# Kernel optimization log

Hardware: AMD Instinct MI355X
Metric: run time of the kernel (lower is better)

Reference implementation:

```python
import jax, jax.numpy as jnp
import numpy as np

E, K, H, I = 64, 8, 2048, 768  # num_experts, top_k, hidden, moe_intermediate

def setup_inputs() -> dict:
    key = jax.random.key(0)
    k1, k2, k3, k4 = jax.random.split(key, 4)
    return {
        "hidden_states": jax.random.normal(k1, (1, 1024, H), dtype=jnp.float32),
        "w_gate": jax.random.normal(k2, (H, E), dtype=jnp.float32) * 0.02,
        "w13": jax.random.normal(k3, (E, H, 2 * I), dtype=jnp.float32) * 0.02,  # fused gate+up proj
        "w2": jax.random.normal(k4, (E, I, H), dtype=jnp.float32) * 0.02,
    }

def reference(hidden_states, w_gate, w13, w2):
    orig_shape = hidden_states.shape
    x = hidden_states.reshape(-1, orig_shape[-1])            # [T, H]
    T = x.shape[0]

    # Router: logits -> softmax -> top-k -> renormalize (norm_topk_prob=True)
    router_logits = x @ w_gate                               # [T, E]
    probs = jax.nn.softmax(router_logits, axis=-1)
    topk_w, topk_idx = jax.lax.top_k(probs, K)               # [T, K]
    topk_w = topk_w / jnp.sum(topk_w, axis=-1, keepdims=True)
    # Dense combine-weight matrix [T, E] (zero for non-routed experts)
    combine = jnp.zeros((T, E), dtype=x.dtype).at[
        jnp.arange(T)[:, None], topk_idx].add(topk_w)

    # Expert SwiGLU FFN, computed densely for all experts, masked by combine
    h = jnp.einsum('th,ehd->etd', x, w13)                    # [E, T, 2I]
    gate, up = h[..., :I], h[..., I:]
    act = jax.nn.silu(gate) * up                             # [E, T, I]
    y = jnp.einsum('eti,eih->eth', act, w2)                  # [E, T, H]
    out = jnp.einsum('eth,te->th', y, combine)               # [T, H]
    return out.reshape(orig_shape)
```

## Files before the change

### kernel.cpp

```cpp
#include <hip/hip_runtime.h>
#include <hip/hip_bf16.h>
#include <math.h>

#define NE 64
#define NK 8
#define NH 2048
#define NI 768
#define NT 1024
#define BP 40
#define SUB64 (64 * BP)
#define SUB128 (128 * BP)

typedef float f32x4 __attribute__((ext_vector_type(4)));
typedef __bf16 bf16x8 __attribute__((ext_vector_type(8)));
typedef __bf16 bf16x4 __attribute__((ext_vector_type(4)));

__global__ __launch_bounds__(256) void router_k(
    const float* __restrict__ x, const float* __restrict__ wg,
    __bf16* __restrict__ x_bf, int* __restrict__ topk_idx,
    float* __restrict__ topk_w)
{
    __shared__ float xs[4][NH];
    const int wave = threadIdx.x >> 6;
    const int lane = threadIdx.x & 63;
    const int t = blockIdx.x * 4 + wave;

    const float* xrow = x + (size_t)t * NH;
    __bf16* brow = x_bf + (size_t)t * NH;
    #pragma unroll
    for (int j = 0; j < 8; ++j) {
        int idx = j * 256 + lane * 4;
        f32x4 v = *reinterpret_cast<const f32x4*>(xrow + idx);
        *reinterpret_cast<f32x4*>(&xs[wave][idx]) = v;
        bf16x4 b;
        b[0] = (__bf16)v.x; b[1] = (__bf16)v.y; b[2] = (__bf16)v.z; b[3] = (__bf16)v.w;
        *reinterpret_cast<bf16x4*>(brow + idx) = b;
    }
    __syncthreads();

    float a0 = 0.f, a1 = 0.f, a2 = 0.f, a3 = 0.f;
    for (int h = 0; h < NH; h += 4) {
        a0 = fmaf(xs[wave][h + 0], wg[(h + 0) * NE + lane], a0);
        a1 = fmaf(xs[wave][h + 1], wg[(h + 1) * NE + lane], a1);
        a2 = fmaf(xs[wave][h + 2], wg[(h + 2) * NE + lane], a2);
        a3 = fmaf(xs[wave][h + 3], wg[(h + 3) * NE + lane], a3);
    }
    float acc = (a0 + a1) + (a2 + a3);

    float cur = acc;
    float sel_v[NK]; int sel_i[NK];
    #pragma unroll
    for (int k = 0; k < NK; ++k) {
        float bv = cur; int bi = lane;
        #pragma unroll
        for (int s = 32; s; s >>= 1) {
            float ov = __shfl_xor(bv, s, 64);
            int   oi = __shfl_xor(bi, s, 64);
            if (ov > bv || (ov == bv && oi < bi)) { bv = ov; bi = oi; }
        }
        sel_v[k] = bv; sel_i[k] = bi;
        if (lane == bi) cur = -3.4e38f;
    }
    float m = sel_v[0];
    float ssum = 0.f;
    #pragma unroll
    for (int k = 0; k < NK; ++k) ssum += expf(sel_v[k] - m);

    if (lane < NK) {
        float w = expf(sel_v[lane] - m) / ssum;
        topk_idx[t * NK + lane] = sel_i[lane];
        topk_w[t * NK + lane] = w;
    }
}

__global__ __launch_bounds__(1024) void scanscatter_k(
    const int* __restrict__ topk_idx, const float* __restrict__ topk_w,
    int* __restrict__ counts, int* __restrict__ offs,
    int* __restrict__ slot_tok, float* __restrict__ slot_w,
    int* __restrict__ slot_of)
{
    __shared__ int hist[NE], base[NE], cur[NE];
    const int tid = threadIdx.x;
    if (tid < NE) hist[tid] = 0;
    __syncthreads();
    for (int i = tid; i < NT * NK; i += 1024)
        atomicAdd(&hist[topk_idx[i]], 1);
    __syncthreads();
    if (tid == 0) {
        int r = 0;
        for (int e = 0; e < NE; ++e) { base[e] = r; r += hist[e]; }
    }
    __syncthreads();
    if (tid < NE) { counts[tid] = hist[tid]; offs[tid] = base[tid]; cur[tid] = 0; }
    __syncthreads();
    for (int i = tid; i < NT * NK; i += 1024) {
        int e = topk_idx[i];
        int p = atomicAdd(&cur[e], 1);
        int g = base[e] + p;
        slot_tok[g] = i >> 3;
        slot_w[g] = topk_w[i];
        slot_of[i] = g;
    }
}

__global__ __launch_bounds__(256, 3) void e1_k(
    const __bf16* __restrict__ x_bf, const float* __restrict__ w13,
    const int* __restrict__ counts, const int* __restrict__ offs,
    const int* __restrict__ slot_tok, __bf16* __restrict__ act)
{
    const int e = blockIdx.x;
    const int cnt = counts[e];
    const int m0 = blockIdx.z * 256;
    if (m0 >= cnt) return;
    const int rows = min(256, cnt - m0);
    const int n0 = blockIdx.y * 32;
    const int goff = offs[e] + m0;

    __shared__ __bf16 B[2][2 * SUB64];
    __shared__ int tok[256];

    const int tid = threadIdx.x;
    tok[tid] = (tid < rows) ? slot_tok[goff + tid] : slot_tok[goff];
    __syncthreads();

    const int wave = tid >> 6, lane = tid & 63;
    f32x4 acc[4][4];
    #pragma unroll
    for (int i = 0; i < 4; ++i)
        #pragma unroll
        for (int j = 0; j < 4; ++j) acc[i][j] = (f32x4){0.f, 0.f, 0.f, 0.f};

    const __bf16* ap[4];
    bool mok[4];
    #pragma unroll
    for (int mf = 0; mf < 4; ++mf) {
        int rf = mf * 64 + wave * 16;
        mok[mf] = (rf < rows);
        int arow = rf + (lane & 15);
        ap[mf] = x_bf + (size_t)tok[arow] * NH + ((lane >> 4) << 3);
    }

    const float* w13e = w13 + (size_t)e * NH * (2 * NI);
    const int cc = tid & 15, kch = tid >> 4;
    const int bcol0 = cc * 4;
    const int gcol = (bcol0 < 32) ? (n0 + bcol0) : (NI + n0 + bcol0 - 32);
    const int rot = (cc >> 1) & 3;
    const float* bptr = w13e + (size_t)(kch * 4) * (2 * NI) + gcol;
    const int sub = kch >> 3, kloc = kch & 7;
    int bj[4], boff[4];
    #pragma unroll
    for (int jj = 0; jj < 4; ++jj) {
        int j = (jj + rot) & 3;
        bj[jj] = j;
        boff[jj] = sub * SUB64 + (bcol0 + j) * BP + kloc * 4;
    }

    f32x4 bReg[4];
    auto loadT = [&](int kk) {
        #pragma unroll
        for (int ki = 0; ki < 4; ++ki)
            bReg[ki] = __builtin_nontemporal_load(
                reinterpret_cast<const f32x4*>(bptr + (size_t)(kk + ki) * (2 * NI)));
    };
    auto writeT = [&](int buf) {
        #pragma unroll
        for (int jj = 0; jj < 4; ++jj) {
            int j = bj[jj];
            bf16x4 p;
            p[0] = (__bf16)bReg[0][j]; p[1] = (__bf16)bReg[1][j];
            p[2] = (__bf16)bReg[2][j]; p[3] = (__bf16)bReg[3][j];
            *reinterpret_cast<bf16x4*>(&B[buf][boff[jj]]) = p;
        }
    };
    auto compute = [&](int buf) {
        #pragma unroll
        for (int kk = 0; kk < 2; ++kk) {
            bf16x8 av[4];
            #pragma unroll
            for (int mf = 0; mf < 4; ++mf)
                if (mok[mf]) av[mf] = *reinterpret_cast<const bf16x8*>(ap[mf] + kk * 32);
            bf16x8 bfr[4];
            #pragma unroll
            for (int nf = 0; nf < 4; ++nf) {
                int col = nf * 16 + (lane & 15);
                bfr[nf] = *reinterpret_cast<const bf16x8*>(
                    &B[buf][kk * SUB64 + col * BP + ((lane >> 4) << 3)]);
            }
            #pragma unroll
            for (int mf = 0; mf < 4; ++mf)
                if (mok[mf])
                    #pragma unroll
                    for (int nf = 0; nf < 4; ++nf)
                        acc[mf][nf] = __builtin_amdgcn_mfma_f32_16x16x32_bf16(
                            av[mf], bfr[nf], acc[mf][nf], 0, 0, 0);
        }
        #pragma unroll
        for (int mf = 0; mf < 4; ++mf) ap[mf] += 64;
    };

    loadT(0);
    writeT(0);
    __syncthreads();

    #pragma unroll 1
    for (int t = 0; t < 32; ++t) {
        if (t + 1 < 32) loadT((t + 1) * 64);
        compute(t & 1);
        if (t + 1 < 32) writeT((t + 1) & 1);
        __syncthreads();
    }

    #pragma unroll
    for (int mf = 0; mf < 4; ++mf) {
        int rf = mf * 64 + wave * 16;
        if (rf >= rows) continue;
        #pragma unroll
        for (int nf = 0; nf < 2; ++nf) {
            f32x4 g = acc[mf][nf];
            f32x4 u = acc[mf][nf + 2];
            int col = n0 + nf * 16 + (lane & 15);
            #pragma unroll
            for (int r = 0; r < 4; ++r) {
                int row = rf + ((lane >> 4) << 2) + r;
                if (row < rows) {
                    float gv = g[r];
                    float a = gv / (1.f + expf(-gv)) * u[r];
                    act[(size_t)(goff + row) * NI + col] = (__bf16)a;
                }
            }
        }
    }
}

__global__ __launch_bounds__(256, 2) void e2_k(
    const __bf16* __restrict__ act, const float* __restrict__ w2,
    const int* __restrict__ counts, const int* __restrict__ offs,
    const float* __restrict__ slot_w, __bf16* __restrict__ partial)
{
    const int e = blockIdx.x;
    const int cnt = counts[e];
    const int m0 = blockIdx.z * 256;
    if (m0 >= cnt) return;
    const int rows = min(256, cnt - m0);
    const int n0 = blockIdx.y * 128;
    const int goff = offs[e] + m0;

    __shared__ __bf16 B[2][2 * SUB128];

    const int tid = threadIdx.x, wave = tid >> 6, lane = tid & 63;
    f32x4 acc[4][8];
    #pragma unroll
    for (int i = 0; i < 4; ++i)
        #pragma unroll
        for (int j = 0; j < 8; ++j) acc[i][j] = (f32x4){0.f, 0.f, 0.f, 0.f};

    const __bf16* ap[4];
    bool mok[4];
    #pragma unroll
    for (int mf = 0; mf < 4; ++mf) {
        int rf = mf * 64 + wave * 16;
        mok[mf] = (rf < rows);
        int arow = goff + rf + (lane & 15);
        ap[mf] = act + (size_t)arow * NI + ((lane >> 4) << 3);
    }

    const float* w2e = w2 + (size_t)e * NI * NH;
    const int cc = tid & 31, kch = tid >> 5;
    const int bcol0 = cc * 4;
    const int rot = (cc >> 1) & 3;
    const float* bptr = w2e + (size_t)(kch * 4) * NH + n0 + bcol0;
    int bj[4], boff[4];
    #pragma unroll
    for (int jj = 0; jj < 4; ++jj) {
        int j = (jj + rot) & 3;
        bj[jj] = j;
        boff[jj] = (bcol0 + j) * BP + kch * 4;
    }

    f32x4 bReg[2][4];
    auto loadT = [&](int kk) {
        #pragma unroll
        for (int s = 0; s < 2; ++s)
            #pragma unroll
            for (int ki = 0; ki < 4; ++ki)
                bReg[s][ki] = __builtin_nontemporal_load(
                    reinterpret_cast<const f32x4*>(bptr + (size_t)(kk + s * 32 + ki) * NH));
    };
    auto writeT = [&](int buf) {
        #pragma unroll
        for (int s = 0; s < 2; ++s)
            #pragma unroll
            for (int jj = 0; jj < 4; ++jj) {
                int j = bj[jj];
                bf16x4 p;
                p[0] = (__bf16)bReg[s][0][j]; p[1] = (__bf16)bReg[s][1][j];
                p[2] = (__bf16)bReg[s][2][j]; p[3] = (__bf16)bReg[s][3][j];
                *reinterpret_cast<bf16x4*>(&B[buf][s * SUB128 + boff[jj]]) = p;
            }
    };
    auto compute = [&](int buf) {
        #pragma unroll
        for (int kk = 0; kk < 2; ++kk) {
            bf16x8 av[4];
            #pragma unroll
            for (int mf = 0; mf < 4; ++mf)
                if (mok[mf]) av[mf] = *reinterpret_cast<const bf16x8*>(ap[mf] + kk * 32);
            bf16x8 bfr[8];
            #pragma unroll
            for (int nf = 0; nf < 8; ++nf) {
                int col = nf * 16 + (lane & 15);
                bfr[nf] = *reinterpret_cast<const bf16x8*>(
                    &B[buf][kk * SUB128 + col * BP + ((lane >> 4) << 3)]);
            }
            #pragma unroll
            for (int mf = 0; mf < 4; ++mf)
                if (mok[mf])
                    #pragma unroll
                    for (int nf = 0; nf < 8; ++nf)
                        acc[mf][nf] = __builtin_amdgcn_mfma_f32_16x16x32_bf16(
                            av[mf], bfr[nf], acc[mf][nf], 0, 0, 0);
        }
        #pragma unroll
        for (int mf = 0; mf < 4; ++mf) ap[mf] += 64;
    };

    loadT(0);
    writeT(0);
    __syncthreads();

    #pragma unroll 1
    for (int t = 0; t < 12; ++t) {
        if (t + 1 < 12) loadT((t + 1) * 64);
        compute(t & 1);
        if (t + 1 < 12) writeT((t + 1) & 1);
        __syncthreads();
    }

    #pragma unroll
    for (int mf = 0; mf < 4; ++mf) {
        int rf = mf * 64 + wave * 16;
        if (rf >= rows) continue;
        int rb = rf + ((lane >> 4) << 2);
        #pragma unroll
        for (int r = 0; r < 4; ++r) {
            int row = rb + r;
            if (row >= rows) continue;
            int gs = goff + row;
            float wv = slot_w[gs];
            #pragma unroll
            for (int nf = 0; nf < 8; ++nf) {
                int col = n0 + nf * 16 + (lane & 15);
                partial[(size_t)gs * NH + col] = (__bf16)(wv * acc[mf][nf][r]);
            }
        }
    }
}

__global__ __launch_bounds__(256) void combine_k(
    const __bf16* __restrict__ partial, const int* __restrict__ slot_of,
    float* __restrict__ out)
{
    const int t = blockIdx.x;
    const int c0 = threadIdx.x * 8;
    __shared__ int gs[NK];
    if (threadIdx.x < NK) gs[threadIdx.x] = slot_of[t * NK + threadIdx.x];
    __syncthreads();

    float s[8] = {0.f, 0.f, 0.f, 0.f, 0.f, 0.f, 0.f, 0.f};
    #pragma unroll
    for (int k = 0; k < NK; ++k) {
        bf16x8 v = *reinterpret_cast<const bf16x8*>(partial + (size_t)gs[k] * NH + c0);
        #pragma unroll
        for (int j = 0; j < 8; ++j) s[j] += (float)v[j];
    }
    f32x4 o0 = {s[0], s[1], s[2], s[3]};
    f32x4 o1 = {s[4], s[5], s[6], s[7]};
    *reinterpret_cast<f32x4*>(out + (size_t)t * NH + c0) = o0;
    *reinterpret_cast<f32x4*>(out + (size_t)t * NH + c0 + 4) = o1;
}

extern "C" void kernel_launch(void* const* d_in, const int* in_sizes, int n_in,
                              void* d_out, int out_size, void* d_ws, size_t ws_size,
                              hipStream_t stream)
{
    const float* x   = (const float*)d_in[0];
    const float* wg  = (const float*)d_in[1];
    const float* w13 = (const float*)d_in[2];
    const float* w2  = (const float*)d_in[3];
    float* out = (float*)d_out;
    char* ws = (char*)d_ws;

    __bf16* x_bf = (__bf16*)ws;
    size_t o = (size_t)4 * 1024 * 1024;
    __bf16* act = (__bf16*)(ws + o);      o += (size_t)8192 * NI * 2;
    __bf16* partial = (__bf16*)(ws + o);  o += (size_t)8192 * NH * 2;
    int*   topk_idx = (int*)(ws + o);     o += 8192 * 4;
    float* topk_w   = (float*)(ws + o);   o += 8192 * 4;
    int*   slot_tok = (int*)(ws + o);     o += 8192 * 4;
    float* slot_w   = (float*)(ws + o);   o += 8192 * 4;
    int*   slot_of  = (int*)(ws + o);     o += 8192 * 4;
    int*   counts   = (int*)(ws + o);     o += 256;
    int*   offs     = (int*)(ws + o);     o += 256;

    router_k    <<<NT / 4, 256, 0, stream>>>(x, wg, x_bf, topk_idx, topk_w);
    scanscatter_k<<<1, 1024, 0, stream>>>(topk_idx, topk_w, counts, offs,
                                          slot_tok, slot_w, slot_of);
    e1_k<<<dim3(NE, NI / 32, 2), 256, 0, stream>>>(x_bf, w13, counts, offs, slot_tok, act);
    e2_k<<<dim3(NE, NH / 128, 2), 256, 0, stream>>>(act, w2, counts, offs, slot_w, partial);
    combine_k<<<NT, 256, 0, stream>>>(partial, slot_of, out);
}
```

Baseline: 396.6 us.

## Split expert GEMM tiles across 8 waves in a 4x2 grid

Both expert GEMM kernels now run 512 threads per block arranged as 4 M-waves by 2 N-waves, so each wave holds half as many accumulators and B fragments. In e1 only the first 256 threads load and convert weights. In e2 the weight loading is spread over all 512 threads, with a new sub/kloc smem offset. The aim is to cut per-wave register pressure and raise occupancy and latency hiding, at the cost of more LDS reads per MFMA and more waves sharing each barrier.

```diff
diff --git a/kernel.cpp b/kernel.cpp
--- a/kernel.cpp
+++ b/kernel.cpp
@@ -103,7 +103,7 @@
     }
 }
 
-__global__ __launch_bounds__(256, 3) void e1_k(
+__global__ __launch_bounds__(512, 4) void e1_k(
     const __bf16* __restrict__ x_bf, const float* __restrict__ w13,
     const int* __restrict__ counts, const int* __restrict__ offs,
     const int* __restrict__ slot_tok, __bf16* __restrict__ act)
@@ -120,28 +120,32 @@
     __shared__ int tok[256];
 
     const int tid = threadIdx.x;
-    tok[tid] = (tid < rows) ? slot_tok[goff + tid] : slot_tok[goff];
+    if (tid < 256) tok[tid] = (tid < rows) ? slot_tok[goff + tid] : slot_tok[goff];
     __syncthreads();
 
     const int wave = tid >> 6, lane = tid & 63;
-    f32x4 acc[4][4];
-    #pragma unroll
-    for (int i = 0; i < 4; ++i)
-        #pragma unroll
-        for (int j = 0; j < 4; ++j) acc[i][j] = (f32x4){0.f, 0.f, 0.f, 0.f};
+    const int wm = wave >> 1, wn = wave & 1;
+
+    f32x4 acc[4][2];
+    #pragma unroll
+    for (int i = 0; i < 4; ++i) {
+        acc[i][0] = (f32x4){0.f, 0.f, 0.f, 0.f};
+        acc[i][1] = (f32x4){0.f, 0.f, 0.f, 0.f};
+    }
 
     const __bf16* ap[4];
     bool mok[4];
     #pragma unroll
-    for (int mf = 0; mf < 4; ++mf) {
-        int rf = mf * 64 + wave * 16;
-        mok[mf] = (rf < rows);
+    for (int fi = 0; fi < 4; ++fi) {
+        int rf = wm * 64 + fi * 16;
+        mok[fi] = (rf < rows);
         int arow = rf + (lane & 15);
-        ap[mf] = x_bf + (size_t)tok[arow] * NH + ((lane >> 4) << 3);
-    }
-
+        ap[fi] = x_bf + (size_t)tok[arow] * NH + ((lane >> 4) << 3);
+    }
+
+    const bool doB = (tid < 256);
     const float* w13e = w13 + (size_t)e * NH * (2 * NI);
-    const int cc = tid & 15, kch = tid >> 4;
+    const int cc = tid & 15, kch = (tid >> 4) & 15;
     const int bcol0 = cc * 4;
     const int gcol = (bcol0 < 32) ? (n0 + bcol0) : (NI + n0 + bcol0 - 32);
     const int rot = (cc >> 1) & 3;
@@ -157,45 +161,47 @@
 
     f32x4 bReg[4];
     auto loadT = [&](int kk) {
-        #pragma unroll
-        for (int ki = 0; ki < 4; ++ki)
-            bReg[ki] = __builtin_nontemporal_load(
-                reinterpret_cast<const f32x4*>(bptr + (size_t)(kk + ki) * (2 * NI)));
+        if (doB)
+            #pragma unroll
+            for (int ki = 0; ki < 4; ++ki)
+                bReg[ki] = __builtin_nontemporal_load(
+                    reinterpret_cast<const f32x4*>(bptr + (size_t)(kk + ki) * (2 * NI)));
     };
     auto writeT = [&](int buf) {
-        #pragma unroll
-        for (int jj = 0; jj < 4; ++jj) {
-            int j = bj[jj];
-            bf16x4 p;
-            p[0] = (__bf16)bReg[0][j]; p[1] = (__bf16)bReg[1][j];
-            p[2] = (__bf16)bReg[2][j]; p[3] = (__bf16)bReg[3][j];
-            *reinterpret_cast<bf16x4*>(&B[buf][boff[jj]]) = p;
-        }
+        if (doB)
+            #pragma unroll
+            for (int jj = 0; jj < 4; ++jj) {
+                int j = bj[jj];
+                bf16x4 p;
+                p[0] = (__bf16)bReg[0][j]; p[1] = (__bf16)bReg[1][j];
+                p[2] = (__bf16)bReg[2][j]; p[3] = (__bf16)bReg[3][j];
+                *reinterpret_cast<bf16x4*>(&B[buf][boff[jj]]) = p;
+            }
     };
     auto compute = [&](int buf) {
         #pragma unroll
         for (int kk = 0; kk < 2; ++kk) {
             bf16x8 av[4];
             #pragma unroll
-            for (int mf = 0; mf < 4; ++mf)
-                if (mok[mf]) av[mf] = *reinterpret_cast<const bf16x8*>(ap[mf] + kk * 32);
-            bf16x8 bfr[4];
-            #pragma unroll
-            for (int nf = 0; nf < 4; ++nf) {
-                int col = nf * 16 + (lane & 15);
-                bfr[nf] = *reinterpret_cast<const bf16x8*>(
-                    &B[buf][kk * SUB64 + col * BP + ((lane >> 4) << 3)]);
-            }
-            #pragma unroll
-            for (int mf = 0; mf < 4; ++mf)
-                if (mok[mf])
-                    #pragma unroll
-                    for (int nf = 0; nf < 4; ++nf)
-                        acc[mf][nf] = __builtin_amdgcn_mfma_f32_16x16x32_bf16(
-                            av[mf], bfr[nf], acc[mf][nf], 0, 0, 0);
-        }
-        #pragma unroll
-        for (int mf = 0; mf < 4; ++mf) ap[mf] += 64;
+            for (int fi = 0; fi < 4; ++fi)
+                if (mok[fi]) av[fi] = *reinterpret_cast<const bf16x8*>(ap[fi] + kk * 32);
+            const int cg = wn * 16 + (lane & 15);
+            const int cu = 32 + wn * 16 + (lane & 15);
+            bf16x8 bg = *reinterpret_cast<const bf16x8*>(
+                &B[buf][kk * SUB64 + cg * BP + ((lane >> 4) << 3)]);
+            bf16x8 bu = *reinterpret_cast<const bf16x8*>(
+                &B[buf][kk * SUB64 + cu * BP + ((lane >> 4) << 3)]);
+            #pragma unroll
+            for (int fi = 0; fi < 4; ++fi)
+                if (mok[fi]) {
+                    acc[fi][0] = __builtin_amdgcn_mfma_f32_16x16x32_bf16(
+                        av[fi], bg, acc[fi][0], 0, 0, 0);
+                    acc[fi][1] = __builtin_amdgcn_mfma_f32_16x16x32_bf16(
+                        av[fi], bu, acc[fi][1], 0, 0, 0);
+                }
+        }
+        #pragma unroll
+        for (int fi = 0; fi < 4; ++fi) ap[fi] += 64;
     };
 
     loadT(0);
@@ -211,28 +217,25 @@
     }
 
     #pragma unroll
-    for (int mf = 0; mf < 4; ++mf) {
-        int rf = mf * 64 + wave * 16;
+    for (int fi = 0; fi < 4; ++fi) {
+        int rf = wm * 64 + fi * 16;
         if (rf >= rows) continue;
-        #pragma unroll
-        for (int nf = 0; nf < 2; ++nf) {
-            f32x4 g = acc[mf][nf];
-            f32x4 u = acc[mf][nf + 2];
-            int col = n0 + nf * 16 + (lane & 15);
-            #pragma unroll
-            for (int r = 0; r < 4; ++r) {
-                int row = rf + ((lane >> 4) << 2) + r;
-                if (row < rows) {
-                    float gv = g[r];
-                    float a = gv / (1.f + expf(-gv)) * u[r];
-                    act[(size_t)(goff + row) * NI + col] = (__bf16)a;
-                }
+        f32x4 g = acc[fi][0];
+        f32x4 u = acc[fi][1];
+        int col = n0 + wn * 16 + (lane & 15);
+        #pragma unroll
+        for (int r = 0; r < 4; ++r) {
+            int row = rf + ((lane >> 4) << 2) + r;
+            if (row < rows) {
+                float gv = g[r];
+                float a = gv / (1.f + expf(-gv)) * u[r];
+                act[(size_t)(goff + row) * NI + col] = (__bf16)a;
             }
         }
     }
 }
 
-__global__ __launch_bounds__(256, 2) void e2_k(
+__global__ __launch_bounds__(512, 4) void e2_k(
     const __bf16* __restrict__ act, const float* __restrict__ w2,
     const int* __restrict__ counts, const int* __restrict__ offs,
     const float* __restrict__ slot_w, __bf16* __restrict__ partial)
@@ -248,80 +251,79 @@
     __shared__ __bf16 B[2][2 * SUB128];
 
     const int tid = threadIdx.x, wave = tid >> 6, lane = tid & 63;
-    f32x4 acc[4][8];
+    const int wm = wave >> 1, wn = wave & 1;
+
+    f32x4 acc[4][4];
     #pragma unroll
     for (int i = 0; i < 4; ++i)
         #pragma unroll
-        for (int j = 0; j < 8; ++j) acc[i][j] = (f32x4){0.f, 0.f, 0.f, 0.f};
+        for (int j = 0; j < 4; ++j) acc[i][j] = (f32x4){0.f, 0.f, 0.f, 0.f};
 
     const __bf16* ap[4];
     bool mok[4];
     #pragma unroll
-    for (int mf = 0; mf < 4; ++mf) {
-        int rf = mf * 64 + wave * 16;
-        mok[mf] = (rf < rows);
+    for (int fi = 0; fi < 4; ++fi) {
+        int rf = wm * 64 + fi * 16;
+        mok[fi] = (rf < rows);
         int arow = goff + rf + (lane & 15);
-        ap[mf] = act + (size_t)arow * NI + ((lane >> 4) << 3);
+        ap[fi] = act + (size_t)arow * NI + ((lane >> 4) << 3);
     }
 
     const float* w2e = w2 + (size_t)e * NI * NH;
-    const int cc = tid & 31, kch = tid >> 5;
+    const int cc = tid & 31, kch = (tid >> 5) & 15;
     const int bcol0 = cc * 4;
     const int rot = (cc >> 1) & 3;
     const float* bptr = w2e + (size_t)(kch * 4) * NH + n0 + bcol0;
+    const int sub = kch >> 3, kloc = kch & 7;
     int bj[4], boff[4];
     #pragma unroll
     for (int jj = 0; jj < 4; ++jj) {
         int j = (jj + rot) & 3;
         bj[jj] = j;
-        boff[jj] = (bcol0 + j) * BP + kch * 4;
-    }
-
-    f32x4 bReg[2][4];
+        boff[jj] = sub * SUB128 + (bcol0 + j) * BP + kloc * 4;
+    }
+
+    f32x4 bReg[4];
     auto loadT = [&](int kk) {
         #pragma unroll
-        for (int s = 0; s < 2; ++s)
-            #pragma unroll
-            for (int ki = 0; ki < 4; ++ki)
-                bReg[s][ki] = __builtin_nontemporal_load(
-                    reinterpret_cast<const f32x4*>(bptr + (size_t)(kk + s * 32 + ki) * NH));
+        for (int ki = 0; ki < 4; ++ki)
+            bReg[ki] = __builtin_nontemporal_load(
+                reinterpret_cast<const f32x4*>(bptr + (size_t)(kk + ki) * NH));
     };
     auto writeT = [&](int buf) {
         #pragma unroll
-        for (int s = 0; s < 2; ++s)
-            #pragma unroll
-            for (int jj = 0; jj < 4; ++jj) {
-                int j = bj[jj];
-                bf16x4 p;
-                p[0] = (__bf16)bReg[s][0][j]; p[1] = (__bf16)bReg[s][1][j];
-                p[2] = (__bf16)bReg[s][2][j]; p[3] = (__bf16)bReg[s][3][j];
-                *reinterpret_cast<bf16x4*>(&B[buf][s * SUB128 + boff[jj]]) = p;
-            }
+        for (int jj = 0; jj < 4; ++jj) {
+            int j = bj[jj];
+            bf16x4 p;
+            p[0] = (__bf16)bReg[0][j]; p[1] = (__bf16)bReg[1][j];
+            p[2] = (__bf16)bReg[2][j]; p[3] = (__bf16)bReg[3][j];
+            *reinterpret_cast<bf16x4*>(&B[buf][boff[jj]]) = p;
+        }
     };
     auto compute = [&](int buf) {
         #pragma unroll
         for (int kk = 0; kk < 2; ++kk) {
             bf16x8 av[4];
             #pragma unroll
-            for (int mf = 0; mf < 4; ++mf)
-                if (mok[mf]) av[mf] = *reinterpret_cast<const bf16x8*>(ap[mf] + kk * 32);
-            bf16x8 bfr[8];
-            #pragma unroll
-            for (int nf = 0; nf < 8; ++nf) {
-                int col = nf * 16 + (lane & 15);
+            for (int fi = 0; fi < 4; ++fi)
+                if (mok[fi]) av[fi] = *reinterpret_cast<const bf16x8*>(ap[fi] + kk * 32);
+            bf16x8 bfr[4];
+            #pragma unroll
+            for (int nf = 0; nf < 4; ++nf) {
+                int col = wn * 64 + nf * 16 + (lane & 15);
                 bfr[nf] = *reinterpret_cast<const bf16x8*>(
                     &B[buf][kk * SUB128 + col * BP + ((lane >> 4) << 3)]);
             }
             #pragma unroll
-            for (int mf = 0; mf < 4; ++mf)
-                if (mok[mf])
+            for (int fi = 0; fi < 4; ++fi)
+                if (mok[fi])
                     #pragma unroll
-                    for (int nf = 0; nf < 8; ++nf)
-                        acc[mf][nf] = __builtin_amdgcn_mfma_f32_16x16x32_bf16(
-                            av[mf], bfr[nf], acc[mf][nf], 0, 0, 0);
-        }
-        #pragma unroll
-        for (int mf = 0; mf < 4; ++mf) ap[mf] += 64;
+                    for (int nf = 0; nf < 4; ++nf)
+                        acc[fi][nf] = __builtin_amdgcn_mfma_f32_16x16x32_bf16(
+                            av[fi], bfr[nf], acc[fi][nf], 0, 0, 0);
+        }
+        #pragma unroll
+        for (int fi = 0; fi < 4; ++fi) ap[fi] += 64;
     };
 
     loadT(0);
@@ -337,8 +339,8 @@
     }
 
     #pragma unroll
-    for (int mf = 0; mf < 4; ++mf) {
-        int rf = mf * 64 + wave * 16;
+    for (int fi = 0; fi < 4; ++fi) {
+        int rf = wm * 64 + fi * 16;
         if (rf >= rows) continue;
         int rb = rf + ((lane >> 4) << 2);
         #pragma unroll
@@ -348,9 +350,9 @@
             int gs = goff + row;
             float wv = slot_w[gs];
             #pragma unroll
-            for (int nf = 0; nf < 8; ++nf) {
-                int col = n0 + nf * 16 + (lane & 15);
-                partial[(size_t)gs * NH + col] = (__bf16)(wv * acc[mf][nf][r]);
+            for (int nf = 0; nf < 4; ++nf) {
+                int col = n0 + wn * 64 + nf * 16 + (lane & 15);
+                partial[(size_t)gs * NH + col] = (__bf16)(wv * acc[fi][nf][r]);
             }
         }
     }
@@ -405,7 +407,7 @@
     router_k    <<<NT / 4, 256, 0, stream>>>(x, wg, x_bf, topk_idx, topk_w);
     scanscatter_k<<<1, 1024, 0, stream>>>(topk_idx, topk_w, counts, offs,
                                           slot_tok, slot_w, slot_of);
-    e1_k<<<dim3(NE, NI / 32, 2), 256, 0, stream>>>(x_bf, w13, counts, offs, slot_tok, act);
-    e2_k<<<dim3(NE, NH / 128, 2), 256, 0, stream>>>(act, w2, counts, offs, slot_w, partial);
+    e1_k<<<dim3(NE, 24, 2), 512, 0, stream>>>(x_bf, w13, counts, offs, slot_tok, act);
+    e2_k<<<dim3(NE, 16, 2), 512, 0, stream>>>(act, w2, counts, offs, slot_w, partial);
     combine_k<<<NT, 256, 0, stream>>>(partial, slot_of, out);
 }
```

Result: slower. 533.5 us (+34.5%).

## Stage router weights in LDS and loop M-tiles inside expert GEMM blocks

Applied to the files above, without the earlier changes.

The router kernel now cooperatively stages 128-row chunks of the gate weight matrix into shared memory instead of every wave reading it from global memory. The expert GEMM kernels drop the z-dimension grid split over 256-row token chunks and instead loop over chunks inside one block, so blocks for lightly loaded experts no longer launch and exit empty. The trade-off is less parallelism when an expert gets more than 256 tokens, since those chunks now run one after another. The weight tile is also reloaded from global memory for each chunk.

```diff
diff --git a/kernel.cpp b/kernel.cpp
--- a/kernel.cpp
+++ b/kernel.cpp
@@ -21,8 +21,10 @@
     float* __restrict__ topk_w)
 {
     __shared__ float xs[4][NH];
-    const int wave = threadIdx.x >> 6;
-    const int lane = threadIdx.x & 63;
+    __shared__ float wgs[128][NE];
+    const int tid = threadIdx.x;
+    const int wave = tid >> 6;
+    const int lane = tid & 63;
     const int t = blockIdx.x * 4 + wave;
 
     const float* xrow = x + (size_t)t * NH;
@@ -36,14 +38,24 @@
         b[0] = (__bf16)v.x; b[1] = (__bf16)v.y; b[2] = (__bf16)v.z; b[3] = (__bf16)v.w;
         *reinterpret_cast<bf16x4*>(brow + idx) = b;
     }
-    __syncthreads();
 
     float a0 = 0.f, a1 = 0.f, a2 = 0.f, a3 = 0.f;
-    for (int h = 0; h < NH; h += 4) {
-        a0 = fmaf(xs[wave][h + 0], wg[(h + 0) * NE + lane], a0);
-        a1 = fmaf(xs[wave][h + 1], wg[(h + 1) * NE + lane], a1);
-        a2 = fmaf(xs[wave][h + 2], wg[(h + 2) * NE + lane], a2);
-        a3 = fmaf(xs[wave][h + 3], wg[(h + 3) * NE + lane], a3);
+    for (int h0 = 0; h0 < NH; h0 += 128) {
+        __syncthreads();
+        #pragma unroll
+        for (int i = 0; i < 32; ++i) {
+            int idx = i * 256 + tid;
+            int r = idx >> 6, c = idx & 63;
+            wgs[r][c] = wg[(size_t)(h0 + r) * NE + c];
+        }
+        __syncthreads();
+        #pragma unroll 8
+        for (int h = 0; h < 128; h += 4) {
+            a0 = fmaf(xs[wave][h0 + h + 0], wgs[h + 0][lane], a0);
+            a1 = fmaf(xs[wave][h0 + h + 1], wgs[h + 1][lane], a1);
+            a2 = fmaf(xs[wave][h0 + h + 2], wgs[h + 2][lane], a2);
+            a3 = fmaf(xs[wave][h0 + h + 3], wgs[h + 3][lane], a3);
+        }
     }
     float acc = (a0 + a1) + (a2 + a3);
 
@@ -110,35 +122,14 @@
 {
     const int e = blockIdx.x;
     const int cnt = counts[e];
-    const int m0 = blockIdx.z * 256;
-    if (m0 >= cnt) return;
-    const int rows = min(256, cnt - m0);
     const int n0 = blockIdx.y * 32;
-    const int goff = offs[e] + m0;
+    const int eoff = offs[e];
 
     __shared__ __bf16 B[2][2 * SUB64];
     __shared__ int tok[256];
 
     const int tid = threadIdx.x;
-    tok[tid] = (tid < rows) ? slot_tok[goff + tid] : slot_tok[goff];
-    __syncthreads();
-
     const int wave = tid >> 6, lane = tid & 63;
-    f32x4 acc[4][4];
-    #pragma unroll
-    for (int i = 0; i < 4; ++i)
-        #pragma unroll
-        for (int j = 0; j < 4; ++j) acc[i][j] = (f32x4){0.f, 0.f, 0.f, 0.f};
-
-    const __bf16* ap[4];
-    bool mok[4];
-    #pragma unroll
-    for (int mf = 0; mf < 4; ++mf) {
-        int rf = mf * 64 + wave * 16;
-        mok[mf] = (rf < rows);
-        int arow = rf + (lane & 15);
-        ap[mf] = x_bf + (size_t)tok[arow] * NH + ((lane >> 4) << 3);
-    }
 
     const float* w13e = w13 + (size_t)e * NH * (2 * NI);
     const int cc = tid & 15, kch = tid >> 4;
@@ -172,60 +163,86 @@
             *reinterpret_cast<bf16x4*>(&B[buf][boff[jj]]) = p;
         }
     };
-    auto compute = [&](int buf) {
-        #pragma unroll
-        for (int kk = 0; kk < 2; ++kk) {
-            bf16x8 av[4];
-            #pragma unroll
-            for (int mf = 0; mf < 4; ++mf)
-                if (mok[mf]) av[mf] = *reinterpret_cast<const bf16x8*>(ap[mf] + kk * 32);
-            bf16x8 bfr[4];
-            #pragma unroll
-            for (int nf = 0; nf < 4; ++nf) {
-                int col = nf * 16 + (lane & 15);
-                bfr[nf] = *reinterpret_cast<const bf16x8*>(
-                    &B[buf][kk * SUB64 + col * BP + ((lane >> 4) << 3)]);
+
+    for (int m0 = 0; m0 < cnt; m0 += 256) {
+        const int rows = min(256, cnt - m0);
+        const int goff = eoff + m0;
+
+        __syncthreads();
+        tok[tid] = (tid < rows) ? slot_tok[goff + tid] : slot_tok[goff];
+        __syncthreads();
+
+        f32x4 acc[4][4];
+        #pragma unroll
+        for (int i = 0; i < 4; ++i)
+            #pragma unroll
+            for (int j = 0; j < 4; ++j) acc[i][j] = (f32x4){0.f, 0.f, 0.f, 0.f};
+
+        const __bf16* ap[4];
+        bool mok[4];
+        #pragma unroll
+        for (int mf = 0; mf < 4; ++mf) {
+            int rf = mf * 64 + wave * 16;
+            mok[mf] = (rf < rows);
+            int arow = rf + (lane & 15);
+            ap[mf] = x_bf + (size_t)tok[arow] * NH + ((lane >> 4) << 3);
+        }
+
+        auto compute = [&](int buf) {
+            #pragma unroll
+            for (int kk = 0; kk < 2; ++kk) {
+                bf16x8 av[4];
+                #pragma unroll
+                for (int mf = 0; mf < 4; ++mf)
+                    if (mok[mf]) av[mf] = *reinterpret_cast<const bf16x8*>(ap[mf] + kk * 32);
+                bf16x8 bfr[4];
+                #pragma unroll
+                for (int nf = 0; nf < 4; ++nf) {
+                    int col = nf * 16 + (lane & 15);
+                    bfr[nf] = *reinterpret_cast<const bf16x8*>(
+                        &B[buf][kk * SUB64 + col * BP + ((lane >> 4) << 3)]);
+                }
+                #pragma unroll
+                for (int mf = 0; mf < 4; ++mf)
+                    if (mok[mf])
+                        #pragma unroll
+                        for (int nf = 0; nf < 4; ++nf)
+                            acc[mf][nf] = __builtin_amdgcn_mfma_f32_16x16x32_bf16(
+                                av[mf], bfr[nf], acc[mf][nf], 0, 0, 0);
             }
             #pragma unroll
-            for (int mf = 0; mf < 4; ++mf)
-                if (mok[mf])
-                    #pragma unroll
-                    for (int nf = 0; nf < 4; ++nf)
-                        acc[mf][nf] = __builtin_amdgcn_mfma_f32_16x16x32_bf16(
-                            av[mf], bfr[nf], acc[mf][nf], 0, 0, 0);
-        }
-        #pragma unroll
-        for (int mf = 0; mf < 4; ++mf) ap[mf] += 64;
-    };
-
-    loadT(0);
-    writeT(0);
-    __syncthreads();
-
-    #pragma unroll 1
-    for (int t = 0; t < 32; ++t) {
-        if (t + 1 < 32) loadT((t + 1) * 64);
-        compute(t & 1);
-        if (t + 1 < 32) writeT((t + 1) & 1);
-        __syncthreads();
-    }
-
-    #pragma unroll
-    for (int mf = 0; mf < 4; ++mf) {
-        int rf = mf * 64 + wave * 16;
-        if (rf >= rows) continue;
-        #pragma unroll
-        for (int nf = 0; nf < 2; ++nf) {
-            f32x4 g = acc[mf][nf];
-            f32x4 u = acc[mf][nf + 2];
-            int col = n0 + nf * 16 + (lane & 15);
-            #pragma unroll
-            for (int r = 0; r < 4; ++r) {
-                int row = rf + ((lane >> 4) << 2) + r;
-                if (row < rows) {
-                    float gv = g[r];
-                    float a = gv / (1.f + expf(-gv)) * u[r];
-                    act[(size_t)(goff + row) * NI + col] = (__bf16)a;
+            for (int mf = 0; mf < 4; ++mf) ap[mf] += 64;
+        };
+
+        loadT(0);
+        writeT(0);
+        __syncthreads();
+
+        #pragma unroll 1
+        for (int t = 0; t < 32; ++t) {
+            if (t + 1 < 32) loadT((t + 1) * 64);
+            compute(t & 1);
+            if (t + 1 < 32) writeT((t + 1) & 1);
+            __syncthreads();
+        }
+
+        #pragma unroll
+        for (int mf = 0; mf < 4; ++mf) {
+            int rf = mf * 64 + wave * 16;
+            if (rf >= rows) continue;
+            #pragma unroll
+            for (int nf = 0; nf < 2; ++nf) {
+                f32x4 g = acc[mf][nf];
+                f32x4 u = acc[mf][nf + 2];
+                int col = n0 + nf * 16 + (lane & 15);
+                #pragma unroll
+                for (int r = 0; r < 4; ++r) {
+                    int row = rf + ((lane >> 4) << 2) + r;
+                    if (row < rows) {
+                        float gv = g[r];
+                        float a = gv / (1.f + expf(-gv)) * u[r];
+                        act[(size_t)(goff + row) * NI + col] = (__bf16)a;
+                    }
                 }
             }
         }
@@ -239,30 +256,12 @@
 {
     const int e = blockIdx.x;
     const int cnt = counts[e];
-    const int m0 = blockIdx.z * 256;
-    if (m0 >= cnt) return;
-    const int rows = min(256, cnt - m0);
     const int n0 = blockIdx.y * 128;
-    const int goff = offs[e] + m0;
+    const int eoff = offs[e];
 
     __shared__ __bf16 B[2][2 * SUB128];
 
     const int tid = threadIdx.x, wave = tid >> 6, lane = tid & 63;
-    f32x4 acc[4][8];
-    #pragma unroll
-    for (int i = 0; i < 4; ++i)
-        #pragma unroll
-        for (int j = 0; j < 8; ++j) acc[i][j] = (f32x4){0.f, 0.f, 0.f, 0.f};
-
-    const __bf16* ap[4];
-    bool mok[4];
-    #pragma unroll
-    for (int mf = 0; mf < 4; ++mf) {
-        int rf = mf * 64 + wave * 16;
-        mok[mf] = (rf < rows);
-        int arow = goff + rf + (lane & 15);
-        ap[mf] = act + (size_t)arow * NI + ((lane >> 4) << 3);
-    }
 
     const float* w2e = w2 + (size_t)e * NI * NH;
     const int cc = tid & 31, kch = tid >> 5;
@@ -298,59 +297,82 @@
                 *reinterpret_cast<bf16x4*>(&B[buf][s * SUB128 + boff[jj]]) = p;
             }
     };
-    auto compute = [&](int buf) {
-        #pragma unroll
-        for (int kk = 0; kk < 2; ++kk) {
-            bf16x8 av[4];
-            #pragma unroll
-            for (int mf = 0; mf < 4; ++mf)
-                if (mok[mf]) av[mf] = *reinterpret_cast<const bf16x8*>(ap[mf] + kk * 32);
-            bf16x8 bfr[8];
-            #pragma unroll
-            for (int nf = 0; nf < 8; ++nf) {
-                int col = nf * 16 + (lane & 15);
-                bfr[nf] = *reinterpret_cast<const bf16x8*>(
-                    &B[buf][kk * SUB128 + col * BP + ((lane >> 4) << 3)]);
+
+    for (int m0 = 0; m0 < cnt; m0 += 256) {
+        const int rows = min(256, cnt - m0);
+        const int goff = eoff + m0;
+
+        f32x4 acc[4][8];
+        #pragma unroll
+        for (int i = 0; i < 4; ++i)
+            #pragma unroll
+            for (int j = 0; j < 8; ++j) acc[i][j] = (f32x4){0.f, 0.f, 0.f, 0.f};
+
+        const __bf16* ap[4];
+        bool mok[4];
+        #pragma unroll
+        for (int mf = 0; mf < 4; ++mf) {
+            int rf = mf * 64 + wave * 16;
+            mok[mf] = (rf < rows);
+            int arow = goff + rf + (lane & 15);
+            ap[mf] = act + (size_t)arow * NI + ((lane >> 4) << 3);
+        }
+
+        auto compute = [&](int buf) {
+            #pragma unroll
+            for (int kk = 0; kk < 2; ++kk) {
+                bf16x8 av[4];
+                #pragma unroll
+                for (int mf = 0; mf < 4; ++mf)
+                    if (mok[mf]) av[mf] = *reinterpret_cast<const bf16x8*>(ap[mf] + kk * 32);
+                bf16x8 bfr[8];
+                #pragma unroll
+                for (int nf = 0; nf < 8; ++nf) {
+                    int col = nf * 16 + (lane & 15);
+                    bfr[nf] = *reinterpret_cast<const bf16x8*>(
+                        &B[buf][kk * SUB128 + col * BP + ((lane >> 4) << 3)]);
+                }
+                #pragma unroll
+                for (int mf = 0; mf < 4; ++mf)
+                    if (mok[mf])
+                        #pragma unroll
+                        for (int nf = 0; nf < 8; ++nf)
+                            acc[mf][nf] = __builtin_amdgcn_mfma_f32_16x16x32_bf16(
+                                av[mf], bfr[nf], acc[mf][nf], 0, 0, 0);
             }
             #pragma unroll
-            for (int mf = 0; mf < 4; ++mf)
-                if (mok[mf])
-                    #pragma unroll
-                    for (int nf = 0; nf < 8; ++nf)
-                        acc[mf][nf] = __builtin_amdgcn_mfma_f32_16x16x32_bf16(
-                            av[mf], bfr[nf], acc[mf][nf], 0, 0, 0);
-        }
-        #pragma unroll
-        for (int mf = 0; mf < 4; ++mf) ap[mf] += 64;
-    };
-
-    loadT(0);
-    writeT(0);
-    __syncthreads();
-
-    #pragma unroll 1
-    for (int t = 0; t < 12; ++t) {
-        if (t + 1 < 12) loadT((t + 1) * 64);
-        compute(t & 1);
-        if (t + 1 < 12) writeT((t + 1) & 1);
-        __syncthreads();
-    }
-
-    #pragma unroll
-    for (int mf = 0; mf < 4; ++mf) {
-        int rf = mf * 64 + wave * 16;
-        if (rf >= rows) continue;
-        int rb = rf + ((lane >> 4) << 2);
-        #pragma unroll
-        for (int r = 0; r < 4; ++r) {
-            int row = rb + r;
-            if (row >= rows) continue;
-            int gs = goff + row;
-            float wv = slot_w[gs];
-            #pragma unroll
-            for (int nf = 0; nf < 8; ++nf) {
-                int col = n0 + nf * 16 + (lane & 15);
-                partial[(size_t)gs * NH + col] = (__bf16)(wv * acc[mf][nf][r]);
+            for (int mf = 0; mf < 4; ++mf) ap[mf] += 64;
+        };
+
+        if (m0) __syncthreads();
+        loadT(0);
+        writeT(0);
+        __syncthreads();
+
+        #pragma unroll 1
+        for (int t = 0; t < 12; ++t) {
+            if (t + 1 < 12) loadT((t + 1) * 64);
+            compute(t & 1);
+            if (t + 1 < 12) writeT((t + 1) & 1);
+            __syncthreads();
+        }
+
+        #pragma unroll
+        for (int mf = 0; mf < 4; ++mf) {
+            int rf = mf * 64 + wave * 16;
+            if (rf >= rows) continue;
+            int rb = rf + ((lane >> 4) << 2);
+            #pragma unroll
+            for (int r = 0; r < 4; ++r) {
+                int row = rb + r;
+                if (row >= rows) continue;
+                int gs = goff + row;
+                float wv = slot_w[gs];
+                #pragma unroll
+                for (int nf = 0; nf < 8; ++nf) {
+                    int col = n0 + nf * 16 + (lane & 15);
+                    partial[(size_t)gs * NH + col] = (__bf16)(wv * acc[mf][nf][r]);
+                }
             }
         }
     }
@@ -405,7 +427,7 @@
     router_k    <<<NT / 4, 256, 0, stream>>>(x, wg, x_bf, topk_idx, topk_w);
     scanscatter_k<<<1, 1024, 0, stream>>>(topk_idx, topk_w, counts, offs,
                                           slot_tok, slot_w, slot_of);
-    e1_k<<<dim3(NE, NI / 32, 2), 256, 0, stream>>>(x_bf, w13, counts, offs, slot_tok, act);
-    e2_k<<<dim3(NE, NH / 128, 2), 256, 0, stream>>>(act, w2, counts, offs, slot_w, partial);
+    e1_k<<<dim3(NE, 24), 256, 0, stream>>>(x_bf, w13, counts, offs, slot_tok, act);
+    e2_k<<<dim3(NE, 16), 256, 0, stream>>>(act, w2, counts, offs, slot_w, partial);
     combine_k<<<NT, 256, 0, stream>>>(partial, slot_of, out);
 }
```

After: 429.8 us. 8.4% more time.
